# Kernel tuning notes

Measured on AMD Instinct MI355X. Metric: run time of the kernel, lower is better.

## Reference

```python
import jax, jax.numpy as jnp
import numpy as np

COUNT_PRIOR_LOG_ODDS = -2.0  # frozen value of exponential_decay(**cfg.OBJ_PRES_COUNT_LOG_PRIOR)
EPS = 1e-9                   # safe_log epsilon
B, H, W = 1024, 16, 16


def setup_inputs() -> dict:
    key = jax.random.key(0)
    k1, k2 = jax.random.split(key)
    z_pres = jax.random.uniform(k1, (B, 1, H, W), dtype=jnp.float32)
    z_pres_prob = jax.random.uniform(k2, (B, 1, H, W), dtype=jnp.float32)
    return {"z_pres": z_pres, "z_pres_prob": z_pres_prob}


def _safe_log(x):
    return jnp.log(x + EPS)


def reference(z_pres, z_pres_prob):
    b, _, h, w = z_pres.shape
    hw = h * w
    s = hw + 1  # count support size

    count_support = jnp.arange(s, dtype=jnp.float32)  # [S]
    p = 1.0 / (jnp.exp(jnp.float32(-COUNT_PRIOR_LOG_ODDS)) + 1.0)
    cd0 = (1.0 - p) * p ** count_support
    cd0 = cd0 / cd0.sum()
    cd0 = jnp.broadcast_to(cd0[None, :], (b, s))      # count_distribution [B, S]
    csf0 = jnp.zeros((b, 1), jnp.float32)             # count_so_far [B, 1]

    # flatten grid in row-major (h, w) order to scan axis: [HW, B, 1]
    probs = z_pres_prob.reshape(b, 1, hw).transpose(2, 0, 1)
    pres = z_pres.reshape(b, 1, hw).transpose(2, 0, 1)
    steps = jnp.arange(hw, dtype=jnp.float32)

    def step(carry, xs):
        cd, csf = carry                 # [B, S], [B, 1]
        prob, zp, i = xs                # [B, 1], [B, 1], scalar
        denom = hw - i
        # P(z=1 | C, z_prev): clamp(count_support - count_so_far, 0, HW - i) / (HW - i)
        p_z_given = jnp.clip(count_support[None, :] - csf, 0.0, denom) / denom  # [B, S]
        p_z = jnp.sum(cd * p_z_given, axis=1, keepdims=True)                    # [B, 1] (the bmm)
        kl = (prob * (_safe_log(prob) - _safe_log(p_z))
              + (1.0 - prob) * (_safe_log(1.0 - prob) - _safe_log(1.0 - p_z)))
        sample = jnp.round(zp)                                                  # [B, 1]
        mult = sample * p_z_given + (1.0 - sample) * (1.0 - p_z_given)          # [B, S]
        cd1 = mult * cd
        norm = jnp.clip(jnp.sum(cd1, axis=1, keepdims=True), 1e-6, None)
        return (cd1 / norm, csf + sample), kl

    (_, _), kls = jax.lax.scan(step, (cd0, csf0), (probs, pres, steps))
    # kls: [HW, B, 1] -> obj_kl [B, 1, H, W]
    return kls.transpose(1, 2, 0).reshape(b, 1, h, w)
```

## Files before the change

kernel.cpp:

```cpp
#include <hip/hip_runtime.h>
#include <math.h>

#define HW 256
#define MINNORM 1.17549435e-38f


template <int CTRL>
__device__ __forceinline__ float dpp_add(float x) {
    int s = __builtin_amdgcn_update_dpp(0, __builtin_bit_cast(int, x),
                                        CTRL, 0xf, 0xf, true);
    return x + __builtin_bit_cast(float, s);
}

__device__ __forceinline__ void row_total2(float x, float y,
                                           float& sx, float& sy) {
    x = dpp_add<0xB1>(x);   y = dpp_add<0xB1>(y);
    x = dpp_add<0x4E>(x);   y = dpp_add<0x4E>(y);
    x = dpp_add<0x128>(x);  y = dpp_add<0x128>(y);
    x = dpp_add<0x124>(x);  y = dpp_add<0x124>(y);
    sx = x; sy = y;
}

__global__ void __launch_bounds__(64, 1)
spair_count_kl(const float* __restrict__ z_pres,
               const float* __restrict__ z_prob,
               float* __restrict__ out) {
    float tok;
    asm volatile("s_setreg_imm32_b32 hwreg(HW_REG_MODE, 4, 2), 0\n\t"
                 "v_mov_b32 %0, 0" : "=v"(tok));

    __shared__ float invt[HW];

    const int lane = threadIdx.x;
    const int l16  = lane & 15;
    const int row  = lane >> 4;
    const int b    = blockIdx.x * 4 + row;

#pragma unroll
    for (int i = 0; i < 4; ++i)
        invt[i * 64 + lane] = 1.0f / (float)(HW - (i * 64 + lane));
    __syncthreads();

    const float e2f = (float)exp(2.0);
    const float pf  = (float)(1.0 / ((double)e2f + 1.0));
    const double pd = (double)pf;
    const double l2p = log2(pd);
    float cd0, cd1, cd2;
    {
        float c[3];
#pragma unroll
        for (int sl = 0; sl < 3; ++sl) {
            const int j = sl * 16 + l16;
            const double powj = exp2((double)j * l2p);
            float v = (float)((1.0 - pd) * powj);
            c[sl] = (v < MINNORM) ? 0.0f : v;
        }
        float ssum = (c[0] + c[1]) + c[2];
        ssum = dpp_add<0xB1>(ssum);  ssum = dpp_add<0x4E>(ssum);
        ssum = dpp_add<0x128>(ssum); ssum = dpp_add<0x124>(ssum);
        cd0 = c[0] / ssum; cd1 = c[1] / ssum; cd2 = c[2] / ssum;
    }
    cd0 += tok; cd1 += tok; cd2 += tok;
    float csf = tok;
    const float jf0 = (float)l16;
    const float jf1 = (float)(16 + l16);
    const float jf2 = (float)(32 + l16);

    const float* presb = z_pres + (size_t)b * HW;
    const float* probb = z_prob + (size_t)b * HW;
    float* outb = out + (size_t)b * HW;

    bool dead = false;

#pragma unroll 1
    for (int k = 0; k < 16; ++k) {
        float mypz = 0.0f;
        float p2last = 0.0f;
        if (!dead) {
#pragma unroll
            for (int c4 = 0; c4 < 4; ++c4) {
                const float4 zp4 = *reinterpret_cast<const float4*>(presb + k * 16 + c4 * 4);
                const float4 iv4 = *reinterpret_cast<const float4*>(&invt[k * 16 + c4 * 4]);
#pragma unroll
                for (int u = 0; u < 4; ++u) {
                    const int ii = c4 * 4 + u;
                    const float zp  = (u == 0) ? zp4.x : (u == 1) ? zp4.y
                                    : (u == 2) ? zp4.z : zp4.w;
                    const float inv = (u == 0) ? iv4.x : (u == 1) ? iv4.y
                                    : (u == 2) ? iv4.z : iv4.w;

                    const float s    = rintf(zp);
                    const float sgn  = fmaf(s, 2.0f, -1.0f);
                    const float base = 1.0f - s;

                    const float t0 = jf0 - csf, t1 = jf1 - csf, t2 = jf2 - csf;
                    const float pg0 = t0 * inv, pg1 = t1 * inv, pg2 = t2 * inv;

                    const float m0 = fmaf(pg0, sgn, base);
                    const float m1 = fmaf(pg1, sgn, base);
                    const float m2 = fmaf(pg2, sgn, base);

                    const float pr0 = cd0 * m0, pr1 = cd1 * m1, pr2 = cd2 * m2;
                    const float y0 = cd0 * pg0, y1 = cd1 * pg1, y2 = cd2 * pg2;

                    float p2, p1s;
                    row_total2((pr0 + pr1) + pr2, (y0 + y1) + y2, p2, p1s);

                    const float norm = fmaxf(p2, 1e-6f);
                    const float invn = __builtin_amdgcn_rcpf(norm);
                    cd0 = pr0 * invn; cd1 = pr1 * invn; cd2 = pr2 * invn;
                    csf += s;

                    const float pz = (s != 0.0f) ? p2 : p1s;
                    mypz = (l16 == ii) ? pz : mypz;
                    p2last = p2;
                }
            }
            if (__ballot(p2last != 0.0f) == 0ULL) dead = true;
        }

        const float prob = probb[k * 16 + l16];
        const float pz = mypz;
        const float kl = prob * (logf(prob + 1e-9f) - logf(pz + 1e-9f))
                       + (1.0f - prob) * (logf((1.0f - prob) + 1e-9f)
                                        - logf((1.0f - pz) + 1e-9f));
        outb[k * 16 + l16] = kl;
    }
}

extern "C" void kernel_launch(void* const* d_in, const int* in_sizes, int n_in,
                              void* d_out, int out_size, void* d_ws, size_t ws_size,
                              hipStream_t stream) {
    const float* z_pres = (const float*)d_in[0];
    const float* z_prob = (const float*)d_in[1];
    float* out = (float*)d_out;
    const int nbatch = in_sizes[0] / HW;
    spair_count_kl<<<dim3(nbatch / 4), dim3(64), 0, stream>>>(z_pres, z_prob, out);
}
```

Baseline: 67.68 us.

## Process two batch rows per lane to interleave independent scan chains

Each wavefront now carries two independent batch elements per 16-lane group, interleaving their serial scan updates and DPP reductions. The aim is to hide the latency of the dependent DPP add chain and rcp by giving the scheduler two independent chains of work. The grid is halved to 128 blocks, which on a GPU with many CUs leaves more of them idle, and the early-exit now requires both chains to be dead.

```diff
diff --git a/kernel.cpp b/kernel.cpp
--- a/kernel.cpp
+++ b/kernel.cpp
@@ -12,13 +12,19 @@
     return x + __builtin_bit_cast(float, s);
 }
 
-__device__ __forceinline__ void row_total2(float x, float y,
-                                           float& sx, float& sy) {
-    x = dpp_add<0xB1>(x);   y = dpp_add<0xB1>(y);
-    x = dpp_add<0x4E>(x);   y = dpp_add<0x4E>(y);
-    x = dpp_add<0x128>(x);  y = dpp_add<0x128>(y);
-    x = dpp_add<0x124>(x);  y = dpp_add<0x124>(y);
-    sx = x; sy = y;
+__device__ __forceinline__ void row_total4(float xa, float ya,
+                                           float xb, float yb,
+                                           float& sxa, float& sya,
+                                           float& sxb, float& syb) {
+    xa = dpp_add<0xB1>(xa);  ya = dpp_add<0xB1>(ya);
+    xb = dpp_add<0xB1>(xb);  yb = dpp_add<0xB1>(yb);
+    xa = dpp_add<0x4E>(xa);  ya = dpp_add<0x4E>(ya);
+    xb = dpp_add<0x4E>(xb);  yb = dpp_add<0x4E>(yb);
+    xa = dpp_add<0x128>(xa); ya = dpp_add<0x128>(ya);
+    xb = dpp_add<0x128>(xb); yb = dpp_add<0x128>(yb);
+    xa = dpp_add<0x124>(xa); ya = dpp_add<0x124>(ya);
+    xb = dpp_add<0x124>(xb); yb = dpp_add<0x124>(yb);
+    sxa = xa; sya = ya; sxb = xb; syb = yb;
 }
 
 __global__ void __launch_bounds__(64, 1)
@@ -34,7 +40,8 @@
     const int lane = threadIdx.x;
     const int l16  = lane & 15;
     const int row  = lane >> 4;
-    const int b    = blockIdx.x * 4 + row;
+    const int bA   = blockIdx.x * 8 + row;
+    const int bB   = bA + 4;
 
 #pragma unroll
     for (int i = 0; i < 4; ++i)
@@ -45,7 +52,7 @@
     const float pf  = (float)(1.0 / ((double)e2f + 1.0));
     const double pd = (double)pf;
     const double l2p = log2(pd);
-    float cd0, cd1, cd2;
+    float cdA0, cdA1, cdA2;
     {
         float c[3];
 #pragma unroll
@@ -58,73 +65,109 @@
         float ssum = (c[0] + c[1]) + c[2];
         ssum = dpp_add<0xB1>(ssum);  ssum = dpp_add<0x4E>(ssum);
         ssum = dpp_add<0x128>(ssum); ssum = dpp_add<0x124>(ssum);
-        cd0 = c[0] / ssum; cd1 = c[1] / ssum; cd2 = c[2] / ssum;
+        cdA0 = c[0] / ssum; cdA1 = c[1] / ssum; cdA2 = c[2] / ssum;
     }
-    cd0 += tok; cd1 += tok; cd2 += tok;
-    float csf = tok;
+    cdA0 += tok; cdA1 += tok; cdA2 += tok;
+    float cdB0 = cdA0, cdB1 = cdA1, cdB2 = cdA2;
+    float csfA = tok, csfB = tok;
     const float jf0 = (float)l16;
     const float jf1 = (float)(16 + l16);
     const float jf2 = (float)(32 + l16);
 
-    const float* presb = z_pres + (size_t)b * HW;
-    const float* probb = z_prob + (size_t)b * HW;
-    float* outb = out + (size_t)b * HW;
+    const float* presA = z_pres + (size_t)bA * HW;
+    const float* probA = z_prob + (size_t)bA * HW;
+    float*       outA  = out    + (size_t)bA * HW;
+    const float* presB = z_pres + (size_t)bB * HW;
+    const float* probB = z_prob + (size_t)bB * HW;
+    float*       outB  = out    + (size_t)bB * HW;
 
     bool dead = false;
 
 #pragma unroll 1
     for (int k = 0; k < 16; ++k) {
-        float mypz = 0.0f;
-        float p2last = 0.0f;
+        float mypzA = 0.0f, mypzB = 0.0f;
+        float p2lA = 0.0f, p2lB = 0.0f;
         if (!dead) {
 #pragma unroll
             for (int c4 = 0; c4 < 4; ++c4) {
-                const float4 zp4 = *reinterpret_cast<const float4*>(presb + k * 16 + c4 * 4);
-                const float4 iv4 = *reinterpret_cast<const float4*>(&invt[k * 16 + c4 * 4]);
+                const float4 zpA4 = *reinterpret_cast<const float4*>(presA + k * 16 + c4 * 4);
+                const float4 zpB4 = *reinterpret_cast<const float4*>(presB + k * 16 + c4 * 4);
+                const float4 iv4  = *reinterpret_cast<const float4*>(&invt[k * 16 + c4 * 4]);
 #pragma unroll
                 for (int u = 0; u < 4; ++u) {
                     const int ii = c4 * 4 + u;
-                    const float zp  = (u == 0) ? zp4.x : (u == 1) ? zp4.y
-                                    : (u == 2) ? zp4.z : zp4.w;
+                    const float zpA = (u == 0) ? zpA4.x : (u == 1) ? zpA4.y
+                                    : (u == 2) ? zpA4.z : zpA4.w;
+                    const float zpB = (u == 0) ? zpB4.x : (u == 1) ? zpB4.y
+                                    : (u == 2) ? zpB4.z : zpB4.w;
                     const float inv = (u == 0) ? iv4.x : (u == 1) ? iv4.y
                                     : (u == 2) ? iv4.z : iv4.w;
 
-                    const float s    = rintf(zp);
-                    const float sgn  = fmaf(s, 2.0f, -1.0f);
-                    const float base = 1.0f - s;
+                    const float sA    = rintf(zpA);
+                    const float sB    = rintf(zpB);
+                    const float sgnA  = fmaf(sA, 2.0f, -1.0f);
+                    const float sgnB  = fmaf(sB, 2.0f, -1.0f);
+                    const float baseA = 1.0f - sA;
+                    const float baseB = 1.0f - sB;
 
-                    const float t0 = jf0 - csf, t1 = jf1 - csf, t2 = jf2 - csf;
-                    const float pg0 = t0 * inv, pg1 = t1 * inv, pg2 = t2 * inv;
+                    const float tA0 = jf0 - csfA, tA1 = jf1 - csfA, tA2 = jf2 - csfA;
+                    const float tB0 = jf0 - csfB, tB1 = jf1 - csfB, tB2 = jf2 - csfB;
+                    const float pgA0 = tA0 * inv, pgA1 = tA1 * inv, pgA2 = tA2 * inv;
+                    const float pgB0 = tB0 * inv, pgB1 = tB1 * inv, pgB2 = tB2 * inv;
 
-                    const float m0 = fmaf(pg0, sgn, base);
-                    const float m1 = fmaf(pg1, sgn, base);
-                    const float m2 = fmaf(pg2, sgn, base);
+                    const float mA0 = fmaf(pgA0, sgnA, baseA);
+                    const float mA1 = fmaf(pgA1, sgnA, baseA);
+                    const float mA2 = fmaf(pgA2, sgnA, baseA);
+                    const float mB0 = fmaf(pgB0, sgnB, baseB);
+                    const float mB1 = fmaf(pgB1, sgnB, baseB);
+                    const float mB2 = fmaf(pgB2, sgnB, baseB);
 
-                    const float pr0 = cd0 * m0, pr1 = cd1 * m1, pr2 = cd2 * m2;
-                    const float y0 = cd0 * pg0, y1 = cd1 * pg1, y2 = cd2 * pg2;
+                    const float prA0 = cdA0 * mA0, prA1 = cdA1 * mA1, prA2 = cdA2 * mA2;
+                    const float prB0 = cdB0 * mB0, prB1 = cdB1 * mB1, prB2 = cdB2 * mB2;
+                    const float yA0 = cdA0 * pgA0, yA1 = cdA1 * pgA1, yA2 = cdA2 * pgA2;
+                    const float yB0 = cdB0 * pgB0, yB1 = cdB1 * pgB1, yB2 = cdB2 * pgB2;
 
-                    float p2, p1s;
-                    row_total2((pr0 + pr1) + pr2, (y0 + y1) + y2, p2, p1s);
+                    float p2A, p1sA, p2B, p1sB;
+                    row_total4((prA0 + prA1) + prA2, (yA0 + yA1) + yA2,
+                               (prB0 + prB1) + prB2, (yB0 + yB1) + yB2,
+                               p2A, p1sA, p2B, p1sB);
 
-                    const float norm = fmaxf(p2, 1e-6f);
-                    const float invn = __builtin_amdgcn_rcpf(norm);
-                    cd0 = pr0 * invn; cd1 = pr1 * invn; cd2 = pr2 * invn;
-                    csf += s;
+                    const float normA = fmaxf(p2A, 1e-6f);
+                    const float normB = fmaxf(p2B, 1e-6f);
+                    const float invnA = __builtin_amdgcn_rcpf(normA);
+                    const float invnB = __builtin_amdgcn_rcpf(normB);
+                    cdA0 = prA0 * invnA; cdA1 = prA1 * invnA; cdA2 = prA2 * invnA;
+                    cdB0 = prB0 * invnB; cdB1 = prB1 * invnB; cdB2 = prB2 * invnB;
+                    csfA += sA;
+                    csfB += sB;
 
-                    const float pz = (s != 0.0f) ? p2 : p1s;
-                    mypz = (l16 == ii) ? pz : mypz;
-                    p2last = p2;
+                    const float pzA = (sA != 0.0f) ? p2A : p1sA;
+                    const float pzB = (sB != 0.0f) ? p2B : p1sB;
+                    mypzA = (l16 == ii) ? pzA : mypzA;
+                    mypzB = (l16 == ii) ? pzB : mypzB;
+                    p2lA = p2A;
+                    p2lB = p2B;
                 }
             }
-            if (__ballot(p2last != 0.0f) == 0ULL) dead = true;
+            if (__ballot((p2lA != 0.0f) || (p2lB != 0.0f)) == 0ULL) dead = true;
         }
 
-        const float prob = probb[k * 16 + l16];
-        const float pz = mypz;
-        const float kl = prob * (logf(prob + 1e-9f) - logf(pz + 1e-9f))
-                       + (1.0f - prob) * (logf((1.0f - prob) + 1e-9f)
-                                        - logf((1.0f - pz) + 1e-9f));
-        outb[k * 16 + l16] = kl;
+        {
+            const float prob = probA[k * 16 + l16];
+            const float pz = mypzA;
+            const float kl = prob * (logf(prob + 1e-9f) - logf(pz + 1e-9f))
+                           + (1.0f - prob) * (logf((1.0f - prob) + 1e-9f)
+                                            - logf((1.0f - pz) + 1e-9f));
+            outA[k * 16 + l16] = kl;
+        }
+        {
+            const float prob = probB[k * 16 + l16];
+            const float pz = mypzB;
+            const float kl = prob * (logf(prob + 1e-9f) - logf(pz + 1e-9f))
+                           + (1.0f - prob) * (logf((1.0f - prob) + 1e-9f)
+                                            - logf((1.0f - pz) + 1e-9f));
+            outB[k * 16 + l16] = kl;
+        }
     }
 }
 
@@ -135,5 +178,5 @@
     const float* z_prob = (const float*)d_in[1];
     float* out = (float*)d_out;
     const int nbatch = in_sizes[0] / HW;
-    spair_count_kl<<<dim3(nbatch / 4), dim3(64), 0, stream>>>(z_pres, z_prob, out);
+    spair_count_kl<<<dim3(nbatch / 8), dim3(64), 0, stream>>>(z_pres, z_prob, out);
 }
```

After: 78.37 us. 15.8% more time.

## Double-buffer z_pres loads and defer KL computation to a separate pass

Applied to the files above, without the earlier changes.

Restructures the serial scan loop to prefetch the next 16-step chunk of z_pres and inverse-denominator values into registers while the current chunk is processed, hiding global and LDS load latency. Per-step p_z values go to a shared buffer, and the log-heavy KL evaluation moves to a second loop after the recurrence, taking it off the serial critical path. When every lane's distribution collapses, the scan exits early and the zero-initialised p_z buffer supplies the remaining values. This costs extra LDS, more live registers for the double buffers, and an added zero-fill pass.

```diff
diff --git a/kernel.cpp b/kernel.cpp
--- a/kernel.cpp
+++ b/kernel.cpp
@@ -30,6 +30,7 @@
                  "v_mov_b32 %0, 0" : "=v"(tok));
 
     __shared__ float invt[HW];
+    __shared__ float pzbuf[4 * 16 * 16];
 
     const int lane = threadIdx.x;
     const int l16  = lane & 15;
@@ -39,6 +40,9 @@
 #pragma unroll
     for (int i = 0; i < 4; ++i)
         invt[i * 64 + lane] = 1.0f / (float)(HW - (i * 64 + lane));
+#pragma unroll
+    for (int i = 0; i < 16; ++i)
+        pzbuf[i * 64 + lane] = 0.0f;
     __syncthreads();
 
     const float e2f = (float)exp(2.0);
@@ -67,60 +71,87 @@
     const float jf2 = (float)(32 + l16);
 
     const float* presb = z_pres + (size_t)b * HW;
+
+    auto do_k = [&](int k, const float4* zp, const float4* iv) -> float {
+        float mypz = 0.0f;
+        float nlast = 0.0f;
+#pragma unroll
+        for (int c4 = 0; c4 < 4; ++c4) {
+            const float4 zp4 = zp[c4];
+            const float4 iv4 = iv[c4];
+#pragma unroll
+            for (int u = 0; u < 4; ++u) {
+                const int ii = c4 * 4 + u;
+                const float zpv = (u == 0) ? zp4.x : (u == 1) ? zp4.y
+                                : (u == 2) ? zp4.z : zp4.w;
+                const float inv = (u == 0) ? iv4.x : (u == 1) ? iv4.y
+                                : (u == 2) ? iv4.z : iv4.w;
+
+                const float s    = rintf(zpv);
+                const float sgn  = fmaf(s, 2.0f, -1.0f);
+                const float base = 1.0f - s;
+
+                const float t0 = jf0 - csf, t1 = jf1 - csf, t2 = jf2 - csf;
+                const float pg0 = t0 * inv, pg1 = t1 * inv, pg2 = t2 * inv;
+
+                const float m0 = fmaf(pg0, sgn, base);
+                const float m1 = fmaf(pg1, sgn, base);
+                const float m2 = fmaf(pg2, sgn, base);
+
+                const float pr0 = cd0 * m0, pr1 = cd1 * m1, pr2 = cd2 * m2;
+                const float y0 = cd0 * pg0, y1 = cd1 * pg1, y2 = cd2 * pg2;
+
+                float p2, p1s;
+                row_total2((pr0 + pr1) + pr2, (y0 + y1) + y2, p2, p1s);
+
+                const float norm = fmaxf(p2, 1e-6f);
+                const float invn = __builtin_amdgcn_rcpf(norm);
+                cd0 = pr0 * invn; cd1 = pr1 * invn; cd2 = pr2 * invn;
+                csf += s;
+
+                const float pz = (s != 0.0f) ? p2 : p1s;
+                mypz = (l16 == ii) ? pz : mypz;
+                nlast = p2;
+            }
+        }
+        pzbuf[(row * 16 + k) * 16 + l16] = mypz;
+        return nlast;
+    };
+
+    float4 zpb0[4], ivb0[4], zpb1[4], ivb1[4];
+#pragma unroll
+    for (int c = 0; c < 4; ++c) {
+        zpb0[c] = *reinterpret_cast<const float4*>(presb + c * 4);
+        ivb0[c] = *reinterpret_cast<const float4*>(&invt[c * 4]);
+    }
+
+#pragma unroll 1
+    for (int kk = 0; kk < 8; ++kk) {
+        const int k0 = 2 * kk, k1 = 2 * kk + 1;
+#pragma unroll
+        for (int c = 0; c < 4; ++c) {
+            zpb1[c] = *reinterpret_cast<const float4*>(presb + k1 * 16 + c * 4);
+            ivb1[c] = *reinterpret_cast<const float4*>(&invt[k1 * 16 + c * 4]);
+        }
+        const float n0 = do_k(k0, zpb0, ivb0);
+        if (__ballot(n0 != 0.0f) == 0ULL) break;
+
+        const int kn = (kk < 7) ? (k0 + 2) : 15;
+#pragma unroll
+        for (int c = 0; c < 4; ++c) {
+            zpb0[c] = *reinterpret_cast<const float4*>(presb + kn * 16 + c * 4);
+            ivb0[c] = *reinterpret_cast<const float4*>(&invt[kn * 16 + c * 4]);
+        }
+        const float n1 = do_k(k1, zpb1, ivb1);
+        if (__ballot(n1 != 0.0f) == 0ULL) break;
+    }
+
     const float* probb = z_prob + (size_t)b * HW;
     float* outb = out + (size_t)b * HW;
-
-    bool dead = false;
-
-#pragma unroll 1
+#pragma unroll 2
     for (int k = 0; k < 16; ++k) {
-        float mypz = 0.0f;
-        float p2last = 0.0f;
-        if (!dead) {
-#pragma unroll
-            for (int c4 = 0; c4 < 4; ++c4) {
-                const float4 zp4 = *reinterpret_cast<const float4*>(presb + k * 16 + c4 * 4);
-                const float4 iv4 = *reinterpret_cast<const float4*>(&invt[k * 16 + c4 * 4]);
-#pragma unroll
-                for (int u = 0; u < 4; ++u) {
-                    const int ii = c4 * 4 + u;
-                    const float zp  = (u == 0) ? zp4.x : (u == 1) ? zp4.y
-                                    : (u == 2) ? zp4.z : zp4.w;
-                    const float inv = (u == 0) ? iv4.x : (u == 1) ? iv4.y
-                                    : (u == 2) ? iv4.z : iv4.w;
-
-                    const float s    = rintf(zp);
-                    const float sgn  = fmaf(s, 2.0f, -1.0f);
-                    const float base = 1.0f - s;
-
-                    const float t0 = jf0 - csf, t1 = jf1 - csf, t2 = jf2 - csf;
-                    const float pg0 = t0 * inv, pg1 = t1 * inv, pg2 = t2 * inv;
-
-                    const float m0 = fmaf(pg0, sgn, base);
-                    const float m1 = fmaf(pg1, sgn, base);
-                    const float m2 = fmaf(pg2, sgn, base);
-
-                    const float pr0 = cd0 * m0, pr1 = cd1 * m1, pr2 = cd2 * m2;
-                    const float y0 = cd0 * pg0, y1 = cd1 * pg1, y2 = cd2 * pg2;
-
-                    float p2, p1s;
-                    row_total2((pr0 + pr1) + pr2, (y0 + y1) + y2, p2, p1s);
-
-                    const float norm = fmaxf(p2, 1e-6f);
-                    const float invn = __builtin_amdgcn_rcpf(norm);
-                    cd0 = pr0 * invn; cd1 = pr1 * invn; cd2 = pr2 * invn;
-                    csf += s;
-
-                    const float pz = (s != 0.0f) ? p2 : p1s;
-                    mypz = (l16 == ii) ? pz : mypz;
-                    p2last = p2;
-                }
-            }
-            if (__ballot(p2last != 0.0f) == 0ULL) dead = true;
-        }
-
+        const float pz = pzbuf[(row * 16 + k) * 16 + l16];
         const float prob = probb[k * 16 + l16];
-        const float pz = mypz;
         const float kl = prob * (logf(prob + 1e-9f) - logf(pz + 1e-9f))
                        + (1.0f - prob) * (logf((1.0f - prob) + 1e-9f)
                                         - logf((1.0f - pz) + 1e-9f));
```

After: 65.46 us. 1.03x faster.
